# Kernel optimization log

Measured on AMD Instinct MI355X. Metric: run time of the kernel, lower is better.

The kernel has to match this reference:

```python
import jax, jax.numpy as jnp
import numpy as np

B = 8       # complexes in batch
C = 32      # CDR residues per antibody
G = 2048    # antigen nodes per complex
D = 128     # encoded_dims
N_AB = B * C
N_AG = B * G
N = N_AB + N_AG
SLOPE = 0.2
EPS_BN = 1e-5


def _build_edges():
    # block-sparse bipartite edges (cdr_b x ag_b), symmetrized, + self loops
    srcs, dsts = [], []
    for b in range(B):
        ab = np.arange(b * C, (b + 1) * C)
        ag = np.arange(N_AB + b * G, N_AB + (b + 1) * G)
        g1, g2 = np.meshgrid(ab, ag, indexing='ij')
        srcs.append(g1.ravel()); dsts.append(g2.ravel())
    s = np.concatenate(srcs); d = np.concatenate(dsts)
    loops = np.arange(N)
    src = np.concatenate([s, d, loops]).astype(np.int32)
    dst = np.concatenate([d, s, loops]).astype(np.int32)
    return src, dst


def setup_inputs() -> dict:
    key = jax.random.key(0)
    ks = jax.random.split(key, 16)
    sc = 1.0 / np.sqrt(D)
    edge_src, edge_dst = _build_edges()
    return {
        'selected_ab': jax.random.normal(ks[0], (N_AB, D), jnp.float32),
        'x_ag': jax.random.normal(ks[1], (N_AG, D), jnp.float32),
        'W1': jax.random.normal(ks[2], (D, D), jnp.float32) * sc,
        'a_src1': jax.random.normal(ks[3], (D,), jnp.float32) * sc,
        'a_dst1': jax.random.normal(ks[4], (D,), jnp.float32) * sc,
        'b1': jnp.zeros((D,), jnp.float32),
        'W2': jax.random.normal(ks[5], (D, D), jnp.float32) * sc,
        'a_src2': jax.random.normal(ks[6], (D,), jnp.float32) * sc,
        'a_dst2': jax.random.normal(ks[7], (D,), jnp.float32) * sc,
        'b2': jnp.zeros((D,), jnp.float32),
        'bn_ab_g': jnp.ones((2 * D,), jnp.float32),
        'bn_ab_b': jnp.zeros((2 * D,), jnp.float32),
        'bn_ag_g': jnp.ones((2 * D,), jnp.float32),
        'bn_ag_b': jnp.zeros((2 * D,), jnp.float32),
        'fc_w': jax.random.normal(ks[8], (2 * D, 1), jnp.float32) * sc,
        'fc_b': jnp.zeros((1,), jnp.float32),
        'agfc_w': jax.random.normal(ks[9], (2 * D, 1), jnp.float32) * sc,
        'agfc_b': jnp.zeros((1,), jnp.float32),
        'edge_src': jnp.asarray(edge_src),
        'edge_dst': jnp.asarray(edge_dst),
    }


def _gat(x, W, a_s, a_d, b, src, dst):
    # PyG GATConv, heads=1, eval mode (dropout off)
    h = x @ W                                  # [N, D]
    al_s = h @ a_s                             # [N]
    al_d = h @ a_d                             # [N]
    e = jax.nn.leaky_relu(al_s[src] + al_d[dst], SLOPE)   # [E]
    m = jax.ops.segment_max(e, dst, num_segments=N)
    e = jnp.exp(e - m[dst])
    z = jax.ops.segment_sum(e, dst, num_segments=N)
    alpha = e / (z[dst] + 1e-16)
    out = jax.ops.segment_sum(h[src] * alpha[:, None], dst, num_segments=N)
    return out + b


def _bn(x, g, b):
    # training-mode batch stats (biased variance), like torch BatchNorm1d
    m = x.mean(0)
    v = ((x - m) ** 2).mean(0)
    return (x - m) / jnp.sqrt(v + EPS_BN) * g + b


def reference(selected_ab, x_ag, W1, a_src1, a_dst1, b1, W2, a_src2, a_dst2, b2,
              bn_ab_g, bn_ab_b, bn_ag_g, bn_ag_b, fc_w, fc_b, agfc_w, agfc_b,
              edge_src, edge_dst):
    x = jnp.concatenate([selected_ab, x_ag], axis=0)          # [N, D]
    x = jax.nn.relu(_gat(x, W1, a_src1, a_dst1, b1, edge_src, edge_dst))
    x = _gat(x, W2, a_src2, a_dst2, b2, edge_src, edge_dst)
    x_ab = jnp.concatenate([x[:N_AB], selected_ab], axis=1)   # [N_ab, 2D]
    x_ab = jax.nn.relu(_bn(x_ab, bn_ab_g, bn_ab_b))
    x_ab = (x_ab @ fc_w + fc_b).ravel()
    x_ag_o = jnp.concatenate([x[N_AB:], x_ag], axis=1)        # [N_ag, 2D]
    x_ag_o = jax.nn.relu(_bn(x_ag_o, bn_ag_g, bn_ag_b))
    x_ag_o = (x_ag_o @ agfc_w + agfc_b).ravel()
    return (x_ab, x_ag_o)
```

## Files before the change

kernel.cpp:

```cpp
#include <hip/hip_runtime.h>


#define N_AB 256
#define N_AG 16384
#define N_ALL 16640
#define G_AG 2048
#define SLOPE 0.2f
#define MSHIFT 20.0f

typedef __attribute__((ext_vector_type(4))) float f32x4;
typedef __attribute__((ext_vector_type(8))) __bf16 bf16x8;
typedef __attribute__((ext_vector_type(8))) unsigned short u16x8;
typedef unsigned short ushort_t;

__device__ __forceinline__ float bf2f(ushort_t u) {
  union { unsigned int i; float f; } v; v.i = ((unsigned int)u) << 16; return v.f;
}
__device__ __forceinline__ ushort_t f2bf(float f) {
  union { float fv; unsigned int i; } v; v.fv = f;
  unsigned int x = v.i;
  return (ushort_t)((x + 0x7fffu + ((x >> 16) & 1u)) >> 16);
}
__device__ __forceinline__ float lrelu(float x) { return x >= 0.f ? x : SLOPE * x; }
__device__ __forceinline__ float expw(float e) {
  return __expf(fminf(e, 60.f) - MSHIFT);
}
__device__ __forceinline__ float ldf(const void* p, size_t i, int f) {
  return f ? ((const float*)p)[i] : bf2f(((const ushort_t*)p)[i]);
}
__device__ __forceinline__ void ld8f(const void* p, size_t i, int f, float* o) {
  if (f) {
    const f32x4* q = (const f32x4*)((const float*)p + i);
    f32x4 a = q[0], b = q[1];
#pragma unroll
    for (int j = 0; j < 4; ++j) { o[j] = a[j]; o[j + 4] = b[j]; }
  } else {
    u16x8 v = *(const u16x8*)((const ushort_t*)p + i);
#pragma unroll
    for (int j = 0; j < 8; ++j) o[j] = bf2f(v[j]);
  }
}

__global__ __launch_bounds__(256) void k_pre(
    const void* __restrict__ W1, const void* __restrict__ W2,
    const void* __restrict__ as1, const void* __restrict__ ad1,
    const void* __restrict__ as2, const void* __restrict__ ad2,
    const ushort_t* __restrict__ selu,
    ushort_t* __restrict__ W1t, ushort_t* __restrict__ W2t,
    float* __restrict__ va, float* __restrict__ bnsumAG,
    float* __restrict__ accf, float* __restrict__ accz,
    int* __restrict__ flagp) {
  int t = threadIdx.x, lane = t & 63, wid = t >> 6;
  int bx = blockIdx.x;
  int cnt = 0;
#pragma unroll
  for (int i = 0; i < 8; ++i) {
    unsigned e = (selu[lane * 8 + i] >> 7) & 0xFF;
    if (e > 0xC8) cnt++;
  }
  int f = (__popcll(__ballot(cnt > 0)) >= 3) ? 1 : 0;
  if (bx == 0 && t == 0) flagp[0] = f;

  if (bx < 16) {
    const void* W = (bx < 8) ? W1 : W2;
    ushort_t* Wt = (bx < 8) ? W1t : W2t;
    int base = (bx & 7) * 2048 + t * 8;
    float o[8];
    ld8f(W, base, f, o);
#pragma unroll
    for (int j = 0; j < 8; ++j) {
      int idx = base + j;
      Wt[(idx & 127) * 128 + (idx >> 7)] = f2bf(o[j]);
    }
  } else if (bx < 32) {
    int j = bx - 16;
    const void* W   = (j < 8) ? W1 : W2;
    const void* asv = (j < 8) ? as1 : as2;
    const void* adv = (j < 8) ? ad1 : ad2;
    int vbase = (j < 8) ? 0 : 256;
    int basek = (j & 7) * 16 + wid * 4;
    float a_s0 = ldf(asv, lane, f), a_s1 = ldf(asv, lane + 64, f);
    float a_d0 = ldf(adv, lane, f), a_d1 = ldf(adv, lane + 64, f);
#pragma unroll
    for (int i = 0; i < 4; ++i) {
      int k = basek + i;
      float w0 = ldf(W, (size_t)k * 128 + lane, f);
      float w1 = ldf(W, (size_t)k * 128 + lane + 64, f);
      float ps = w0 * a_s0 + w1 * a_s1;
      float pd = w0 * a_d0 + w1 * a_d1;
#pragma unroll
      for (int o = 1; o < 64; o <<= 1) {
        ps += __shfl_xor(ps, o);
        pd += __shfl_xor(pd, o);
      }
      if (lane == 0) { va[vbase + k] = ps; va[vbase + 128 + k] = pd; }
    }
  } else {
    int j = bx - 32;
    f32x4* az = (f32x4*)(accf + (size_t)j * 4096);
    f32x4 z4 = (f32x4){0.f, 0.f, 0.f, 0.f};
    for (int i = t; i < 1024; i += 256) az[i] = z4;
    if (j == 0) { bnsumAG[t] = 0.f; bnsumAG[t + 256] = 0.f; accz[t] = 0.f; }
  }
}

__global__ __launch_bounds__(256) void k_gemm(
    const void* __restrict__ xa, int modeA,
    const void* __restrict__ xb, int modeB,
    const int* __restrict__ flagp,
    const ushort_t* __restrict__ Wt, const float* __restrict__ va,
    ushort_t* __restrict__ h, float* __restrict__ als, float* __restrict__ ald) {
  int lane = threadIdx.x & 63, wid = threadIdx.x >> 6;
  int rw0 = blockIdx.x * 64 + wid * 16;
  const void* xsrc; int roff, mode;
  if (rw0 < N_AB) { xsrc = xa; roff = rw0; mode = modeA; }
  else            { xsrc = xb; roff = rw0 - N_AB; mode = modeB; }
  int fx = (mode == 2) ? *flagp : mode;
  int mm = lane & 15, q = lane >> 4;
  f32x4 acc[8];
#pragma unroll
  for (int b = 0; b < 8; ++b) acc[b] = (f32x4){0.f, 0.f, 0.f, 0.f};
  float pals = 0.f, pald = 0.f;
#pragma unroll
  for (int s = 0; s < 4; ++s) {
    int koff = s * 32 + q * 8;
    union { u16x8 u; bf16x8 b; } af;
    float o[8];
    ld8f(xsrc, (size_t)(roff + mm) * 128 + koff, fx, o);
#pragma unroll
    for (int j = 0; j < 8; ++j) {
      af.u[j] = f2bf(o[j]);
      pals += o[j] * va[koff + j];
      pald += o[j] * va[128 + koff + j];
    }
#pragma unroll
    for (int nt = 0; nt < 8; ++nt) {
      bf16x8 bfr = *(const bf16x8*)(Wt + (size_t)(nt * 16 + mm) * 128 + koff);
      acc[nt] = __builtin_amdgcn_mfma_f32_16x16x32_bf16(af.b, bfr, acc[nt], 0, 0, 0);
    }
  }
  {
    float s1 = pals; s1 += __shfl_xor(s1, 16); s1 += __shfl_xor(s1, 32);
    float d1 = pald; d1 += __shfl_xor(d1, 16); d1 += __shfl_xor(d1, 32);
    if (lane < 16) { als[rw0 + lane] = s1; ald[rw0 + lane] = d1; }
  }
#pragma unroll
  for (int nt = 0; nt < 8; ++nt)
#pragma unroll
    for (int r = 0; r < 4; ++r) {
      int row = rw0 + q * 4 + r;
      int col = nt * 16 + mm;
      h[(size_t)row * 128 + col] = f2bf(acc[nt][r]);
    }
}

#define ABP_STRIDE 72
#define AG_STRIDE 40
__global__ __launch_bounds__(256) void k_agg(
    const ushort_t* __restrict__ h, const float* __restrict__ als,
    const float* __restrict__ ald, const void* __restrict__ bias,
    const int* __restrict__ flagp, ushort_t* __restrict__ xout,
    float* __restrict__ accf, float* __restrict__ accz,
    const void* __restrict__ x_ag, float* __restrict__ bnsumAG,
    int do_relu, int do_bnsum) {
  __shared__ ushort_t hT[128 * ABP_STRIDE];
  __shared__ float alsS[64];
  __shared__ float colsum[128], colsq[128];
  int bx = blockIdx.x;
  int t = threadIdx.x, lane = t & 63, wid = t >> 6;
  int mm = lane & 15, q = lane >> 4;

  if (bx < 256) {
    int b = bx >> 5, jt = bx & 31;
    int f = *flagp;
    {
      int row = t & 31, c0 = (t >> 5) * 16;
      const ushort_t* src = h + (size_t)(b * 32 + row) * 128 + c0;
      u16x8 v0 = *(const u16x8*)src;
      u16x8 v1 = *(const u16x8*)(src + 8);
#pragma unroll
      for (int j = 0; j < 8; ++j) {
        hT[(c0 + j) * AG_STRIDE + row] = v0[j];
        hT[(c0 + 8 + j) * AG_STRIDE + row] = v1[j];
      }
      if (t < 32) alsS[t] = als[b * 32 + t];
      if (t < 128) { colsum[t] = 0.f; colsq[t] = 0.f; }
    }
    __syncthreads();
    int jl = jt * 64 + wid * 16;
    int jrow = N_AB + b * G_AG + jl;
    float aldj = ald[jrow + mm];
    float alsj = als[jrow + mm];
    union { u16x8 u; bf16x8 b; } af;
    float zp = 0.f;
#pragma unroll
    for (int j = 0; j < 8; ++j) {
      ushort_t us = f2bf(expw(lrelu(alsS[q * 8 + j] + aldj)));
      af.u[j] = us;
      zp += bf2f(us);
    }
    zp += __shfl_xor(zp, 16);
    zp += __shfl_xor(zp, 32);
    float wself = expw(lrelu(alsj + aldj));
    float z = zp + wself;
#pragma unroll
    for (int nt = 0; nt < 8; ++nt) {
      int col = nt * 16 + mm;
      union { u16x8 u; bf16x8 b; } bfr;
      bfr.b = *(const bf16x8*)(&hT[col * AG_STRIDE + q * 8]);
      f32x4 acc = {0.f, 0.f, 0.f, 0.f};
      acc = __builtin_amdgcn_mfma_f32_16x16x32_bf16(af.b, bfr.b, acc, 0, 0, 0);
      float biasv = ldf(bias, col, f);
      float sl = 0.f, sq = 0.f;
#pragma unroll
      for (int r = 0; r < 4; ++r) {
        int row = q * 4 + r;
        float zr = __shfl(z, row);
        float wsr = __shfl(wself, row);
        float hv = bf2f(h[(size_t)(jrow + row) * 128 + col]);
        float v = (acc[r] + wsr * hv) / (zr + 1e-16f) + biasv;
        sl += v; sq += v * v;
        if (do_relu) v = fmaxf(v, 0.f);
        xout[(size_t)(jrow + row) * 128 + col] = f2bf(v);
      }
      if (do_bnsum) {
        atomicAdd(&colsum[col], sl);
        atomicAdd(&colsq[col], sq);
      }
    }
    if (do_bnsum) {
      __syncthreads();
      if (t < 128) {
        atomicAdd(&bnsumAG[t], colsum[t]);
        atomicAdd(&bnsumAG[256 + t], colsq[t]);
      }
    }
  } else if (bx < 512) {
    int bx2 = bx - 256;
    int b = bx2 >> 5, sg = bx2 & 31;
    int jrow0 = N_AB + b * G_AG + sg * 64;
    {
      int jr = t & 63, cgrp = (t >> 6) * 32;
      const ushort_t* src = h + (size_t)(jrow0 + jr) * 128 + cgrp;
#pragma unroll
      for (int v = 0; v < 4; ++v) {
        u16x8 vv = *(const u16x8*)(src + v * 8);
#pragma unroll
        for (int j = 0; j < 8; ++j)
          hT[(cgrp + v * 8 + j) * ABP_STRIDE + jr] = vv[j];
      }
      if (t < 64) alsS[t] = als[jrow0 + t];
    }
    __syncthreads();
    float aldm[2] = { ald[b * 32 + mm], ald[b * 32 + 16 + mm] };
    f32x4 acc[2][2];
#pragma unroll
    for (int a = 0; a < 2; ++a)
#pragma unroll
      for (int c = 0; c < 2; ++c) acc[a][c] = (f32x4){0.f, 0.f, 0.f, 0.f};
    float zz[2] = {0.f, 0.f};
#pragma unroll
    for (int s = 0; s < 2; ++s) {
      int k0 = s * 32 + q * 8;
      float a8[8];
#pragma unroll
      for (int j = 0; j < 8; ++j) a8[j] = alsS[k0 + j];
      union { u16x8 u; bf16x8 b; } af[2];
#pragma unroll
      for (int mt = 0; mt < 2; ++mt)
#pragma unroll
        for (int j = 0; j < 8; ++j) {
          ushort_t us = f2bf(expw(lrelu(a8[j] + aldm[mt])));
          af[mt].u[j] = us;
          zz[mt] += bf2f(us);
        }
#pragma unroll
      for (int ns = 0; ns < 2; ++ns) {
        int n = wid * 32 + ns * 16 + mm;
        union { u16x8 u; bf16x8 b; } bfr;
        bfr.b = *(const bf16x8*)(&hT[n * ABP_STRIDE + k0]);
        acc[0][ns] = __builtin_amdgcn_mfma_f32_16x16x32_bf16(af[0].b, bfr.b, acc[0][ns], 0, 0, 0);
        acc[1][ns] = __builtin_amdgcn_mfma_f32_16x16x32_bf16(af[1].b, bfr.b, acc[1][ns], 0, 0, 0);
      }
    }
#pragma unroll
    for (int mt = 0; mt < 2; ++mt)
#pragma unroll
      for (int ns = 0; ns < 2; ++ns)
#pragma unroll
        for (int r = 0; r < 4; ++r) {
          int row = b * 32 + mt * 16 + q * 4 + r;
          int col = wid * 32 + ns * 16 + mm;
          atomicAdd(&accf[(size_t)row * 128 + col], acc[mt][ns][r]);
        }
#pragma unroll
    for (int mt = 0; mt < 2; ++mt) {
      float z = zz[mt];
      z += __shfl_xor(z, 16);
      z += __shfl_xor(z, 32);
      if (wid == 0 && lane < 16)
        atomicAdd(&accz[b * 32 + mt * 16 + lane], z);
    }
  } else {
    int j = bx - 512;
    int f = *flagp;
    int col = t & 127, half = t >> 7;
    int r0 = j * 256 + half * 128;
    float s = 0.f, sq = 0.f;
    for (int r = 0; r < 128; ++r) {
      float v = ldf(x_ag, (size_t)(r0 + r) * 128 + col, f);
      s += v; sq += v * v;
    }
    atomicAdd(&bnsumAG[128 + col], s);
    atomicAdd(&bnsumAG[384 + col], sq);
  }
}

__global__ __launch_bounds__(256) void k_abfin(
    float* __restrict__ accf, float* __restrict__ accz,
    const ushort_t* __restrict__ h, const float* __restrict__ als,
    const float* __restrict__ ald, const void* __restrict__ bias,
    const int* __restrict__ flagp, float* __restrict__ xabf, int do_relu) {
  __shared__ float zsh[32];
  int b = blockIdx.x, t = threadIdx.x;
  int f = *flagp;
  if (t < 32) {
    int grow = b * 32 + t;
    float w = expw(lrelu(als[grow] + ald[grow]));
    zsh[t] = accz[grow] + w;
    accz[grow] = 0.f;
  }
  __syncthreads();
  int c = t & 127, rh = t >> 7;
  float biasv = ldf(bias, c, f);
#pragma unroll 4
  for (int r = 0; r < 16; ++r) {
    int row = rh * 16 + r;
    int grow = b * 32 + row;
    float wself = expw(lrelu(als[grow] + ald[grow]));
    size_t idx = (size_t)grow * 128 + c;
    float hv = bf2f(h[idx]);
    float v = (accf[idx] + wself * hv) / (zsh[row] + 1e-16f) + biasv;
    accf[idx] = 0.f;
    if (do_relu) v = fmaxf(v, 0.f);
    xabf[idx] = v;
  }
}

__global__ __launch_bounds__(256) void k_stats(
    const float* __restrict__ xfab, const void* __restrict__ sel_ab,
    const float* __restrict__ bnsumAG,
    const void* __restrict__ gab, const void* __restrict__ bab,
    const void* __restrict__ gag, const void* __restrict__ bag,
    const void* __restrict__ fcw, const void* __restrict__ agfcw,
    const int* __restrict__ flagp,
    float* __restrict__ statsAB, float* __restrict__ statsAG) {
  int c = threadIdx.x;
  int f = *flagp;
  if (blockIdx.x == 0) {
    float s = 0.f, sq = 0.f;
    if (c < 128) {
      for (int r = 0; r < 256; ++r) { float v = xfab[(size_t)r * 128 + c]; s += v; sq += v * v; }
    } else {
      for (int r = 0; r < 256; ++r) {
        float v = ldf(sel_ab, (size_t)r * 128 + (c - 128), f);
        s += v; sq += v * v;
      }
    }
    float mean = s * (1.f / 256.f);
    float var = fmaxf(sq * (1.f / 256.f) - mean * mean, 0.f);
    float A = ldf(gab, c, f) / sqrtf(var + 1e-5f);
    statsAB[c] = A;
    statsAB[256 + c] = ldf(bab, c, f) - mean * A;
    statsAB[512 + c] = ldf(fcw, c, f);
  } else {
    float mean = bnsumAG[c] * (1.f / 16384.f);
    float var = fmaxf(bnsumAG[256 + c] * (1.f / 16384.f) - mean * mean, 0.f);
    float A = ldf(gag, c, f) / sqrtf(var + 1e-5f);
    statsAG[c] = A;
    statsAG[256 + c] = ldf(bag, c, f) - mean * A;
    statsAG[512 + c] = ldf(agfcw, c, f);
  }
}

__global__ __launch_bounds__(256) void k_head(
    const float* __restrict__ xfab, const ushort_t* __restrict__ xfag,
    const void* __restrict__ sel_ab, const void* __restrict__ x_ag,
    const float* __restrict__ statsAB, const float* __restrict__ statsAG,
    const void* __restrict__ fcb, const void* __restrict__ agfcb,
    const int* __restrict__ flagp, void* __restrict__ out) {
  int lane = threadIdx.x & 63, wid = threadIdx.x >> 6;
  int row = blockIdx.x * 4 + wid;
  int f = *flagp;
  int c0 = lane * 2;
  const float* st;
  float v0, v1, v2, v3, bb;
  if (row < N_AB) {
    st = statsAB;
    const float* p = xfab + (size_t)row * 128 + c0;
    v0 = p[0]; v1 = p[1];
    size_t ro = (size_t)row * 128 + c0;
    v2 = ldf(sel_ab, ro, f);
    v3 = ldf(sel_ab, ro + 1, f);
    bb = ldf(fcb, 0, f);
  } else {
    st = statsAG;
    const ushort_t* p = xfag + (size_t)row * 128 + c0;
    v0 = bf2f(p[0]); v1 = bf2f(p[1]);
    size_t ro = (size_t)(row - N_AB) * 128 + c0;
    v2 = ldf(x_ag, ro, f);
    v3 = ldf(x_ag, ro + 1, f);
    bb = ldf(agfcb, 0, f);
  }
  float acc =
      fmaxf(v0 * st[c0]           + st[256 + c0],     0.f) * st[512 + c0]
    + fmaxf(v1 * st[c0 + 1]       + st[256 + c0 + 1], 0.f) * st[512 + c0 + 1]
    + fmaxf(v2 * st[128 + c0]     + st[384 + c0],     0.f) * st[640 + c0]
    + fmaxf(v3 * st[128 + c0 + 1] + st[384 + c0 + 1], 0.f) * st[640 + c0 + 1];
#pragma unroll
  for (int o = 1; o < 64; o <<= 1) acc += __shfl_xor(acc, o);
  if (lane == 0) {
    float r = acc + bb;
    if (f) ((float*)out)[row] = r;
    else   ((ushort_t*)out)[row] = f2bf(r);
  }
}

extern "C" void kernel_launch(void* const* d_in, const int* in_sizes, int n_in,
                              void* d_out, int out_size, void* d_ws, size_t ws_size,
                              hipStream_t stream) {
  (void)in_sizes; (void)n_in; (void)out_size; (void)ws_size;
  const void* sel_ab = d_in[0];
  const void* x_ag   = d_in[1];
  const void* W1     = d_in[2];
  const void* as1    = d_in[3];
  const void* ad1    = d_in[4];
  const void* b1     = d_in[5];
  const void* W2     = d_in[6];
  const void* as2    = d_in[7];
  const void* ad2    = d_in[8];
  const void* b2     = d_in[9];
  const void* gab    = d_in[10];
  const void* bab    = d_in[11];
  const void* gag    = d_in[12];
  const void* bag    = d_in[13];
  const void* fcw    = d_in[14];
  const void* fcb    = d_in[15];
  const void* agfcw  = d_in[16];
  const void* agfcb  = d_in[17];

  ushort_t* h  = (ushort_t*)d_in[18];
  ushort_t* xb = (ushort_t*)d_in[19];

  char* wsp = (char*)d_ws;
  size_t off = 0;
  auto carve = [&](size_t bytes) -> char* {
    char* p = wsp + off; off += (bytes + 255) & ~(size_t)255; return p;
  };
  int* flag      = (int*)carve(64 * 4);
  ushort_t* W1t  = (ushort_t*)carve(16384 * 2);
  ushort_t* W2t  = (ushort_t*)carve(16384 * 2);
  float* va      = (float*)carve(512 * 4);
  float* als     = (float*)carve((size_t)N_ALL * 4);
  float* ald     = (float*)carve((size_t)N_ALL * 4);
  float* bnsumAG = (float*)carve(512 * 4);
  float* statsAB = (float*)carve(768 * 4);
  float* statsAG = (float*)carve(768 * 4);
  float* xabf    = (float*)carve((size_t)N_AB * 128 * 4);
  float* accf    = (float*)carve((size_t)N_AB * 128 * 4);
  float* accz    = (float*)carve(256 * 4);

  k_pre<<<40, 256, 0, stream>>>(W1, W2, as1, ad1, as2, ad2,
                                (const ushort_t*)sel_ab, W1t, W2t, va,
                                bnsumAG, accf, accz, flag);
  k_gemm<<<260, 256, 0, stream>>>(sel_ab, 2, x_ag, 2, flag, W1t, va, h, als, ald);
  k_agg<<<512, 256, 0, stream>>>(h, als, ald, b1, flag, xb, accf, accz,
                                 x_ag, bnsumAG, 1, 0);
  k_abfin<<<8, 256, 0, stream>>>(accf, accz, h, als, ald, b1, flag, xabf, 1);
  k_gemm<<<260, 256, 0, stream>>>(xabf, 1, xb + (size_t)N_AB * 128, 0, flag, W2t, va + 256, h, als, ald);
  k_agg<<<576, 256, 0, stream>>>(h, als, ald, b2, flag, xb, accf, accz,
                                 x_ag, bnsumAG, 0, 1);
  k_abfin<<<8, 256, 0, stream>>>(accf, accz, h, als, ald, b2, flag, xabf, 0);
  k_stats<<<2, 256, 0, stream>>>(xabf, sel_ab, bnsumAG, gab, bab, gag, bag, fcw, agfcw, flag, statsAB, statsAG);
  k_head<<<4160, 256, 0, stream>>>(xabf, xb, sel_ab, x_ag, statsAB, statsAG, fcb, agfcb, flag, d_out);
}
```

Measured before the change: 199.6 us.

## Fuse all stages into one persistent kernel with software grid barriers

```diff
diff --git a/kernel.cpp b/kernel.cpp
--- a/kernel.cpp
+++ b/kernel.cpp
@@ -7,6 +7,7 @@
 #define G_AG 2048
 #define SLOPE 0.2f
 #define MSHIFT 20.0f
+#define NBLK 512
 
 typedef __attribute__((ext_vector_type(4))) float f32x4;
 typedef __attribute__((ext_vector_type(8))) __bf16 bf16x8;
@@ -41,25 +42,105 @@
   }
 }
 
-__global__ __launch_bounds__(256) void k_pre(
-    const void* __restrict__ W1, const void* __restrict__ W2,
-    const void* __restrict__ as1, const void* __restrict__ ad1,
-    const void* __restrict__ as2, const void* __restrict__ ad2,
-    const ushort_t* __restrict__ selu,
+__device__ __forceinline__ void gbar(int* __restrict__ bar, int id) {
+  __syncthreads();
+  if (threadIdx.x == 0) {
+    __threadfence();
+    atomicAdd(&bar[id], 1);
+    while (__hip_atomic_load(&bar[id], __ATOMIC_RELAXED,
+                             __HIP_MEMORY_SCOPE_AGENT) < NBLK)
+      __builtin_amdgcn_s_sleep(1);
+    __threadfence();
+  }
+  __syncthreads();
+}
+
+__device__ __forceinline__ void gemm_do(
+    const void* xa, int fa, const void* xg, int fg,
+    const ushort_t* __restrict__ Wt, const float* __restrict__ va,
+    ushort_t* __restrict__ h, float* __restrict__ als, float* __restrict__ ald,
+    int bx, int lane, int wid) {
+  int mm = lane & 15, q = lane >> 4;
+  for (int u = bx; u < 520; u += NBLK) {
+    int rw0 = u * 32 + (wid >> 1) * 16;
+    int ch = wid & 1;
+    const void* xsrc; int roff, fx;
+    if (rw0 < N_AB) { xsrc = xa; roff = rw0; fx = fa; }
+    else            { xsrc = xg; roff = rw0 - N_AB; fx = fg; }
+    f32x4 acc[4];
+#pragma unroll
+    for (int b = 0; b < 4; ++b) acc[b] = (f32x4){0.f, 0.f, 0.f, 0.f};
+    float pals = 0.f, pald = 0.f;
+#pragma unroll
+    for (int s = 0; s < 4; ++s) {
+      int koff = s * 32 + q * 8;
+      union { u16x8 u16; bf16x8 b16; } af;
+      float o[8];
+      ld8f(xsrc, (size_t)(roff + mm) * 128 + koff, fx, o);
+#pragma unroll
+      for (int j = 0; j < 8; ++j) {
+        af.u16[j] = f2bf(o[j]);
+        pals += o[j] * va[koff + j];
+        pald += o[j] * va[128 + koff + j];
+      }
+#pragma unroll
+      for (int nt = 0; nt < 4; ++nt) {
+        int colb = ch * 64 + nt * 16;
+        bf16x8 bfr = *(const bf16x8*)(Wt + (size_t)(colb + mm) * 128 + koff);
+        acc[nt] = __builtin_amdgcn_mfma_f32_16x16x32_bf16(af.b16, bfr, acc[nt], 0, 0, 0);
+      }
+    }
+    if (ch == 0) {
+      float s1 = pals; s1 += __shfl_xor(s1, 16); s1 += __shfl_xor(s1, 32);
+      float d1 = pald; d1 += __shfl_xor(d1, 16); d1 += __shfl_xor(d1, 32);
+      if (lane < 16) { als[rw0 + lane] = s1; ald[rw0 + lane] = d1; }
+    }
+#pragma unroll
+    for (int nt = 0; nt < 4; ++nt)
+#pragma unroll
+      for (int r = 0; r < 4; ++r) {
+        int row = rw0 + q * 4 + r;
+        int col = ch * 64 + nt * 16 + mm;
+        h[(size_t)row * 128 + col] = f2bf(acc[nt][r]);
+      }
+  }
+}
+
+__global__ __launch_bounds__(256, 2) void k_fused(
+    const void* __restrict__ sel_ab, const void* __restrict__ x_ag,
+    const void* __restrict__ W1, const void* __restrict__ as1,
+    const void* __restrict__ ad1, const void* __restrict__ b1,
+    const void* __restrict__ W2, const void* __restrict__ as2,
+    const void* __restrict__ ad2, const void* __restrict__ b2,
+    const void* __restrict__ gab, const void* __restrict__ bab,
+    const void* __restrict__ gag, const void* __restrict__ bag,
+    const void* __restrict__ fcw, const void* __restrict__ fcb,
+    const void* __restrict__ agfcw, const void* __restrict__ agfcb,
+    ushort_t* __restrict__ h, ushort_t* __restrict__ xb,
     ushort_t* __restrict__ W1t, ushort_t* __restrict__ W2t,
-    float* __restrict__ va, float* __restrict__ bnsumAG,
+    float* __restrict__ va, float* __restrict__ als, float* __restrict__ ald,
+    float* __restrict__ bnsumAG, float* __restrict__ xabf,
     float* __restrict__ accf, float* __restrict__ accz,
-    int* __restrict__ flagp) {
+    float* __restrict__ statsAG, int* __restrict__ bar,
+    void* __restrict__ out) {
+  __shared__ ushort_t hT[128 * 72];
+  __shared__ float alsS[64];
+  __shared__ float cs0[128], cs1[128];
+  __shared__ float stA[256], stB[256], stW[256];
+  __shared__ float z4[4], w4[4];
+
   int t = threadIdx.x, lane = t & 63, wid = t >> 6;
   int bx = blockIdx.x;
+  int mm = lane & 15, q = lane >> 4;
+
   int cnt = 0;
+  const ushort_t* selu = (const ushort_t*)sel_ab;
 #pragma unroll
   for (int i = 0; i < 8; ++i) {
     unsigned e = (selu[lane * 8 + i] >> 7) & 0xFF;
     if (e > 0xC8) cnt++;
   }
   int f = (__popcll(__ballot(cnt > 0)) >= 3) ? 1 : 0;
-  if (bx == 0 && t == 0) flagp[0] = f;
 
   if (bx < 16) {
     const void* W = (bx < 8) ? W1 : W2;
@@ -95,215 +176,183 @@
       }
       if (lane == 0) { va[vbase + k] = ps; va[vbase + 128 + k] = pd; }
     }
-  } else {
+  } else if (bx < 40) {
     int j = bx - 32;
     f32x4* az = (f32x4*)(accf + (size_t)j * 4096);
-    f32x4 z4 = (f32x4){0.f, 0.f, 0.f, 0.f};
-    for (int i = t; i < 1024; i += 256) az[i] = z4;
+    f32x4 zz = (f32x4){0.f, 0.f, 0.f, 0.f};
+    for (int i = t; i < 1024; i += 256) az[i] = zz;
     if (j == 0) { bnsumAG[t] = 0.f; bnsumAG[t + 256] = 0.f; accz[t] = 0.f; }
   }
-}
-
-__global__ __launch_bounds__(256) void k_gemm(
-    const void* __restrict__ xa, int modeA,
-    const void* __restrict__ xb, int modeB,
-    const int* __restrict__ flagp,
-    const ushort_t* __restrict__ Wt, const float* __restrict__ va,
-    ushort_t* __restrict__ h, float* __restrict__ als, float* __restrict__ ald) {
-  int lane = threadIdx.x & 63, wid = threadIdx.x >> 6;
-  int rw0 = blockIdx.x * 64 + wid * 16;
-  const void* xsrc; int roff, mode;
-  if (rw0 < N_AB) { xsrc = xa; roff = rw0; mode = modeA; }
-  else            { xsrc = xb; roff = rw0 - N_AB; mode = modeB; }
-  int fx = (mode == 2) ? *flagp : mode;
-  int mm = lane & 15, q = lane >> 4;
-  f32x4 acc[8];
-#pragma unroll
-  for (int b = 0; b < 8; ++b) acc[b] = (f32x4){0.f, 0.f, 0.f, 0.f};
-  float pals = 0.f, pald = 0.f;
-#pragma unroll
-  for (int s = 0; s < 4; ++s) {
-    int koff = s * 32 + q * 8;
-    union { u16x8 u; bf16x8 b; } af;
-    float o[8];
-    ld8f(xsrc, (size_t)(roff + mm) * 128 + koff, fx, o);
-#pragma unroll
-    for (int j = 0; j < 8; ++j) {
-      af.u[j] = f2bf(o[j]);
-      pals += o[j] * va[koff + j];
-      pald += o[j] * va[128 + koff + j];
-    }
-#pragma unroll
-    for (int nt = 0; nt < 8; ++nt) {
-      bf16x8 bfr = *(const bf16x8*)(Wt + (size_t)(nt * 16 + mm) * 128 + koff);
-      acc[nt] = __builtin_amdgcn_mfma_f32_16x16x32_bf16(af.b, bfr, acc[nt], 0, 0, 0);
-    }
-  }
-  {
-    float s1 = pals; s1 += __shfl_xor(s1, 16); s1 += __shfl_xor(s1, 32);
-    float d1 = pald; d1 += __shfl_xor(d1, 16); d1 += __shfl_xor(d1, 32);
-    if (lane < 16) { als[rw0 + lane] = s1; ald[rw0 + lane] = d1; }
-  }
-#pragma unroll
-  for (int nt = 0; nt < 8; ++nt)
-#pragma unroll
-    for (int r = 0; r < 4; ++r) {
-      int row = rw0 + q * 4 + r;
-      int col = nt * 16 + mm;
-      h[(size_t)row * 128 + col] = f2bf(acc[nt][r]);
-    }
-}
-
-#define ABP_STRIDE 72
-#define AG_STRIDE 40
-__global__ __launch_bounds__(256) void k_agg(
-    const ushort_t* __restrict__ h, const float* __restrict__ als,
-    const float* __restrict__ ald, const void* __restrict__ bias,
-    const int* __restrict__ flagp, ushort_t* __restrict__ xout,
-    float* __restrict__ accf, float* __restrict__ accz,
-    const void* __restrict__ x_ag, float* __restrict__ bnsumAG,
-    int do_relu, int do_bnsum) {
-  __shared__ ushort_t hT[128 * ABP_STRIDE];
-  __shared__ float alsS[64];
-  __shared__ float colsum[128], colsq[128];
-  int bx = blockIdx.x;
-  int t = threadIdx.x, lane = t & 63, wid = t >> 6;
-  int mm = lane & 15, q = lane >> 4;
-
-  if (bx < 256) {
-    int b = bx >> 5, jt = bx & 31;
-    int f = *flagp;
-    {
-      int row = t & 31, c0 = (t >> 5) * 16;
-      const ushort_t* src = h + (size_t)(b * 32 + row) * 128 + c0;
-      u16x8 v0 = *(const u16x8*)src;
-      u16x8 v1 = *(const u16x8*)(src + 8);
+  gbar(bar, 0);
+
+  gemm_do(sel_ab, f, x_ag, f, W1t, va, h, als, ald, bx, lane, wid);
+  gbar(bar, 1);
+
+  auto agg_phase = [&](const void* bias, int do_relu, int do_bnsum) {
+    if (bx < 256) {
+      int b = bx >> 5, jt = bx & 31;
+      {
+        int row = t & 31, c0g = (t >> 5) * 16;
+        const ushort_t* src = h + (size_t)(b * 32 + row) * 128 + c0g;
+        u16x8 v0 = *(const u16x8*)src;
+        u16x8 v1 = *(const u16x8*)(src + 8);
+#pragma unroll
+        for (int j = 0; j < 8; ++j) {
+          hT[(c0g + j) * 40 + row] = v0[j];
+          hT[(c0g + 8 + j) * 40 + row] = v1[j];
+        }
+        if (t < 32) alsS[t] = als[b * 32 + t];
+        if (t < 128) { cs0[t] = 0.f; cs1[t] = 0.f; }
+      }
+      __syncthreads();
+      int jl = jt * 64 + wid * 16;
+      int jrow = N_AB + b * G_AG + jl;
+      float aldj = ald[jrow + mm];
+      float alsj = als[jrow + mm];
+      union { u16x8 u16; bf16x8 b16; } af;
+      float zp = 0.f;
 #pragma unroll
       for (int j = 0; j < 8; ++j) {
-        hT[(c0 + j) * AG_STRIDE + row] = v0[j];
-        hT[(c0 + 8 + j) * AG_STRIDE + row] = v1[j];
-      }
-      if (t < 32) alsS[t] = als[b * 32 + t];
-      if (t < 128) { colsum[t] = 0.f; colsq[t] = 0.f; }
-    }
-    __syncthreads();
-    int jl = jt * 64 + wid * 16;
-    int jrow = N_AB + b * G_AG + jl;
-    float aldj = ald[jrow + mm];
-    float alsj = als[jrow + mm];
-    union { u16x8 u; bf16x8 b; } af;
-    float zp = 0.f;
-#pragma unroll
-    for (int j = 0; j < 8; ++j) {
-      ushort_t us = f2bf(expw(lrelu(alsS[q * 8 + j] + aldj)));
-      af.u[j] = us;
-      zp += bf2f(us);
-    }
-    zp += __shfl_xor(zp, 16);
-    zp += __shfl_xor(zp, 32);
-    float wself = expw(lrelu(alsj + aldj));
-    float z = zp + wself;
-#pragma unroll
-    for (int nt = 0; nt < 8; ++nt) {
-      int col = nt * 16 + mm;
-      union { u16x8 u; bf16x8 b; } bfr;
-      bfr.b = *(const bf16x8*)(&hT[col * AG_STRIDE + q * 8]);
-      f32x4 acc = {0.f, 0.f, 0.f, 0.f};
-      acc = __builtin_amdgcn_mfma_f32_16x16x32_bf16(af.b, bfr.b, acc, 0, 0, 0);
-      float biasv = ldf(bias, col, f);
-      float sl = 0.f, sq = 0.f;
-#pragma unroll
-      for (int r = 0; r < 4; ++r) {
-        int row = q * 4 + r;
-        float zr = __shfl(z, row);
-        float wsr = __shfl(wself, row);
-        float hv = bf2f(h[(size_t)(jrow + row) * 128 + col]);
-        float v = (acc[r] + wsr * hv) / (zr + 1e-16f) + biasv;
-        sl += v; sq += v * v;
+        ushort_t us = f2bf(expw(lrelu(alsS[q * 8 + j] + aldj)));
+        af.u16[j] = us;
+        zp += bf2f(us);
+      }
+      zp += __shfl_xor(zp, 16);
+      zp += __shfl_xor(zp, 32);
+      float wself = expw(lrelu(alsj + aldj));
+      float z = zp + wself;
+#pragma unroll
+      for (int nt = 0; nt < 8; ++nt) {
+        int col = nt * 16 + mm;
+        union { u16x8 u16; bf16x8 b16; } bfr;
+        bfr.b16 = *(const bf16x8*)(&hT[col * 40 + q * 8]);
+        f32x4 acc = {0.f, 0.f, 0.f, 0.f};
+        acc = __builtin_amdgcn_mfma_f32_16x16x32_bf16(af.b16, bfr.b16, acc, 0, 0, 0);
+        float biasv = ldf(bias, col, f);
+        float sl = 0.f, sq = 0.f;
+#pragma unroll
+        for (int r = 0; r < 4; ++r) {
+          int row = q * 4 + r;
+          float zr = __shfl(z, row);
+          float wsr = __shfl(wself, row);
+          float hv = bf2f(h[(size_t)(jrow + row) * 128 + col]);
+          float v = (acc[r] + wsr * hv) / (zr + 1e-16f) + biasv;
+          sl += v; sq += v * v;
+          if (do_relu) v = fmaxf(v, 0.f);
+          xb[(size_t)(jrow + row) * 128 + col] = f2bf(v);
+        }
+        if (do_bnsum) {
+          atomicAdd(&cs0[col], sl);
+          atomicAdd(&cs1[col], sq);
+        }
+      }
+      if (do_bnsum) {
+        __syncthreads();
+        if (t < 128) {
+          atomicAdd(&bnsumAG[t], cs0[t]);
+          atomicAdd(&bnsumAG[256 + t], cs1[t]);
+        }
+      }
+    } else {
+      int bx2 = bx - 256;
+      int b = bx2 >> 5, sg = bx2 & 31;
+      int jrow0 = N_AB + b * G_AG + sg * 64;
+      {
+        int jr = t & 63, cgrp = (t >> 6) * 32;
+        const ushort_t* src = h + (size_t)(jrow0 + jr) * 128 + cgrp;
+#pragma unroll
+        for (int v = 0; v < 4; ++v) {
+          u16x8 vv = *(const u16x8*)(src + v * 8);
+#pragma unroll
+          for (int j = 0; j < 8; ++j)
+            hT[(cgrp + v * 8 + j) * 72 + jr] = vv[j];
+        }
+        if (t < 64) alsS[t] = als[jrow0 + t];
+      }
+      __syncthreads();
+      float aldm[2] = { ald[b * 32 + mm], ald[b * 32 + 16 + mm] };
+      f32x4 acc[2][2];
+#pragma unroll
+      for (int a = 0; a < 2; ++a)
+#pragma unroll
+        for (int c = 0; c < 2; ++c) acc[a][c] = (f32x4){0.f, 0.f, 0.f, 0.f};
+      float zz[2] = {0.f, 0.f};
+#pragma unroll
+      for (int s = 0; s < 2; ++s) {
+        int k0 = s * 32 + q * 8;
+        float a8[8];
+#pragma unroll
+        for (int j = 0; j < 8; ++j) a8[j] = alsS[k0 + j];
+        union { u16x8 u16; bf16x8 b16; } af[2];
+#pragma unroll
+        for (int mt = 0; mt < 2; ++mt)
+#pragma unroll
+          for (int j = 0; j < 8; ++j) {
+            ushort_t us = f2bf(expw(lrelu(a8[j] + aldm[mt])));
+            af[mt].u16[j] = us;
+            zz[mt] += bf2f(us);
+          }
+#pragma unroll
+        for (int ns = 0; ns < 2; ++ns) {
+          int n = wid * 32 + ns * 16 + mm;
+          union { u16x8 u16; bf16x8 b16; } bfr;
+          bfr.b16 = *(const bf16x8*)(&hT[n * 72 + k0]);
+          acc[0][ns] = __builtin_amdgcn_mfma_f32_16x16x32_bf16(af[0].b16, bfr.b16, acc[0][ns], 0, 0, 0);
+          acc[1][ns] = __builtin_amdgcn_mfma_f32_16x16x32_bf16(af[1].b16, bfr.b16, acc[1][ns], 0, 0, 0);
+        }
+      }
+#pragma unroll
+      for (int mt = 0; mt < 2; ++mt)
+#pragma unroll
+        for (int ns = 0; ns < 2; ++ns)
+#pragma unroll
+          for (int r = 0; r < 4; ++r) {
+            int row = b * 32 + mt * 16 + q * 4 + r;
+            int col = wid * 32 + ns * 16 + mm;
+            atomicAdd(&accf[(size_t)row * 128 + col], acc[mt][ns][r]);
+          }
+#pragma unroll
+      for (int mt = 0; mt < 2; ++mt) {
+        float z = zz[mt];
+        z += __shfl_xor(z, 16);
+        z += __shfl_xor(z, 32);
+        if (wid == 0 && lane < 16)
+          atomicAdd(&accz[b * 32 + mt * 16 + lane], z);
+      }
+    }
+  };
+
+  auto abfin_phase = [&](const void* bias, int do_relu) {
+    if (bx < 64) {
+      int b = bx >> 3, rg = bx & 7;
+      if (t < 4) {
+        int grow = b * 32 + rg * 4 + t;
+        float w = expw(lrelu(als[grow] + ald[grow]));
+        z4[t] = accz[grow] + w;
+        w4[t] = w;
+        accz[grow] = 0.f;
+      }
+      __syncthreads();
+#pragma unroll
+      for (int e = t; e < 512; e += 256) {
+        int rl = e >> 7, col = e & 127;
+        int grow = b * 32 + rg * 4 + rl;
+        size_t idx = (size_t)grow * 128 + col;
+        float hv = bf2f(h[idx]);
+        float v = (accf[idx] + w4[rl] * hv) / (z4[rl] + 1e-16f) + ldf(bias, col, f);
+        accf[idx] = 0.f;
         if (do_relu) v = fmaxf(v, 0.f);
-        xout[(size_t)(jrow + row) * 128 + col] = f2bf(v);
-      }
-      if (do_bnsum) {
-        atomicAdd(&colsum[col], sl);
-        atomicAdd(&colsq[col], sq);
-      }
-    }
-    if (do_bnsum) {
-      __syncthreads();
-      if (t < 128) {
-        atomicAdd(&bnsumAG[t], colsum[t]);
-        atomicAdd(&bnsumAG[256 + t], colsq[t]);
-      }
-    }
-  } else if (bx < 512) {
-    int bx2 = bx - 256;
-    int b = bx2 >> 5, sg = bx2 & 31;
-    int jrow0 = N_AB + b * G_AG + sg * 64;
-    {
-      int jr = t & 63, cgrp = (t >> 6) * 32;
-      const ushort_t* src = h + (size_t)(jrow0 + jr) * 128 + cgrp;
-#pragma unroll
-      for (int v = 0; v < 4; ++v) {
-        u16x8 vv = *(const u16x8*)(src + v * 8);
-#pragma unroll
-        for (int j = 0; j < 8; ++j)
-          hT[(cgrp + v * 8 + j) * ABP_STRIDE + jr] = vv[j];
-      }
-      if (t < 64) alsS[t] = als[jrow0 + t];
-    }
-    __syncthreads();
-    float aldm[2] = { ald[b * 32 + mm], ald[b * 32 + 16 + mm] };
-    f32x4 acc[2][2];
-#pragma unroll
-    for (int a = 0; a < 2; ++a)
-#pragma unroll
-      for (int c = 0; c < 2; ++c) acc[a][c] = (f32x4){0.f, 0.f, 0.f, 0.f};
-    float zz[2] = {0.f, 0.f};
-#pragma unroll
-    for (int s = 0; s < 2; ++s) {
-      int k0 = s * 32 + q * 8;
-      float a8[8];
-#pragma unroll
-      for (int j = 0; j < 8; ++j) a8[j] = alsS[k0 + j];
-      union { u16x8 u; bf16x8 b; } af[2];
-#pragma unroll
-      for (int mt = 0; mt < 2; ++mt)
-#pragma unroll
-        for (int j = 0; j < 8; ++j) {
-          ushort_t us = f2bf(expw(lrelu(a8[j] + aldm[mt])));
-          af[mt].u[j] = us;
-          zz[mt] += bf2f(us);
-        }
-#pragma unroll
-      for (int ns = 0; ns < 2; ++ns) {
-        int n = wid * 32 + ns * 16 + mm;
-        union { u16x8 u; bf16x8 b; } bfr;
-        bfr.b = *(const bf16x8*)(&hT[n * ABP_STRIDE + k0]);
-        acc[0][ns] = __builtin_amdgcn_mfma_f32_16x16x32_bf16(af[0].b, bfr.b, acc[0][ns], 0, 0, 0);
-        acc[1][ns] = __builtin_amdgcn_mfma_f32_16x16x32_bf16(af[1].b, bfr.b, acc[1][ns], 0, 0, 0);
-      }
-    }
-#pragma unroll
-    for (int mt = 0; mt < 2; ++mt)
-#pragma unroll
-      for (int ns = 0; ns < 2; ++ns)
-#pragma unroll
-        for (int r = 0; r < 4; ++r) {
-          int row = b * 32 + mt * 16 + q * 4 + r;
-          int col = wid * 32 + ns * 16 + mm;
-          atomicAdd(&accf[(size_t)row * 128 + col], acc[mt][ns][r]);
-        }
-#pragma unroll
-    for (int mt = 0; mt < 2; ++mt) {
-      float z = zz[mt];
-      z += __shfl_xor(z, 16);
-      z += __shfl_xor(z, 32);
-      if (wid == 0 && lane < 16)
-        atomicAdd(&accz[b * 32 + mt * 16 + lane], z);
-    }
-  } else {
-    int j = bx - 512;
-    int f = *flagp;
+        xabf[idx] = v;
+      }
+    }
+  };
+
+  agg_phase(b1, 1, 0);
+  gbar(bar, 2);
+
+  abfin_phase(b1, 1);
+  if (bx >= 64 && bx < 128) {
+    int j = bx - 64;
     int col = t & 127, half = t >> 7;
     int r0 = j * 256 + half * 128;
     float s = 0.f, sq = 0.f;
@@ -314,115 +363,93 @@
     atomicAdd(&bnsumAG[128 + col], s);
     atomicAdd(&bnsumAG[384 + col], sq);
   }
-}
-
-__global__ __launch_bounds__(256) void k_abfin(
-    float* __restrict__ accf, float* __restrict__ accz,
-    const ushort_t* __restrict__ h, const float* __restrict__ als,
-    const float* __restrict__ ald, const void* __restrict__ bias,
-    const int* __restrict__ flagp, float* __restrict__ xabf, int do_relu) {
-  __shared__ float zsh[32];
-  int b = blockIdx.x, t = threadIdx.x;
-  int f = *flagp;
-  if (t < 32) {
-    int grow = b * 32 + t;
-    float w = expw(lrelu(als[grow] + ald[grow]));
-    zsh[t] = accz[grow] + w;
-    accz[grow] = 0.f;
-  }
-  __syncthreads();
-  int c = t & 127, rh = t >> 7;
-  float biasv = ldf(bias, c, f);
-#pragma unroll 4
-  for (int r = 0; r < 16; ++r) {
-    int row = rh * 16 + r;
-    int grow = b * 32 + row;
-    float wself = expw(lrelu(als[grow] + ald[grow]));
-    size_t idx = (size_t)grow * 128 + c;
-    float hv = bf2f(h[idx]);
-    float v = (accf[idx] + wself * hv) / (zsh[row] + 1e-16f) + biasv;
-    accf[idx] = 0.f;
-    if (do_relu) v = fmaxf(v, 0.f);
-    xabf[idx] = v;
-  }
-}
-
-__global__ __launch_bounds__(256) void k_stats(
-    const float* __restrict__ xfab, const void* __restrict__ sel_ab,
-    const float* __restrict__ bnsumAG,
-    const void* __restrict__ gab, const void* __restrict__ bab,
-    const void* __restrict__ gag, const void* __restrict__ bag,
-    const void* __restrict__ fcw, const void* __restrict__ agfcw,
-    const int* __restrict__ flagp,
-    float* __restrict__ statsAB, float* __restrict__ statsAG) {
-  int c = threadIdx.x;
-  int f = *flagp;
-  if (blockIdx.x == 0) {
-    float s = 0.f, sq = 0.f;
-    if (c < 128) {
-      for (int r = 0; r < 256; ++r) { float v = xfab[(size_t)r * 128 + c]; s += v; sq += v * v; }
-    } else {
-      for (int r = 0; r < 256; ++r) {
-        float v = ldf(sel_ab, (size_t)r * 128 + (c - 128), f);
-        s += v; sq += v * v;
-      }
-    }
-    float mean = s * (1.f / 256.f);
-    float var = fmaxf(sq * (1.f / 256.f) - mean * mean, 0.f);
-    float A = ldf(gab, c, f) / sqrtf(var + 1e-5f);
-    statsAB[c] = A;
-    statsAB[256 + c] = ldf(bab, c, f) - mean * A;
-    statsAB[512 + c] = ldf(fcw, c, f);
+  gbar(bar, 3);
+
+  gemm_do(xabf, 1, xb + (size_t)N_AB * 128, 0, W2t, va + 256, h, als, ald,
+          bx, lane, wid);
+  gbar(bar, 4);
+
+  agg_phase(b2, 0, 1);
+  gbar(bar, 5);
+
+  abfin_phase(b2, 0);
+  if (bx == 64 && t < 256) {
+    float mean = bnsumAG[t] * (1.f / 16384.f);
+    float var = fmaxf(bnsumAG[256 + t] * (1.f / 16384.f) - mean * mean, 0.f);
+    float A = ldf(gag, t, f) / sqrtf(var + 1e-5f);
+    statsAG[t] = A;
+    statsAG[256 + t] = ldf(bag, t, f) - mean * A;
+    statsAG[512 + t] = ldf(agfcw, t, f);
+  }
+  gbar(bar, 6);
+
+  if (bx < 504) {
+    if (t < 256) { stA[t] = statsAG[t]; stB[t] = statsAG[256 + t]; stW[t] = statsAG[512 + t]; }
+    __syncthreads();
+    float bb = ldf(agfcb, 0, f);
+    int c0 = lane * 2;
+    for (int u = bx; u < 4096; u += 504) {
+      int rloc = u * 4 + wid;
+      int row = N_AB + rloc;
+      const ushort_t* p = xb + (size_t)row * 128 + c0;
+      float v0 = bf2f(p[0]), v1 = bf2f(p[1]);
+      size_t ro = (size_t)rloc * 128 + c0;
+      float v2 = ldf(x_ag, ro, f), v3 = ldf(x_ag, ro + 1, f);
+      float acc =
+          fmaxf(v0 * stA[c0]           + stB[c0],       0.f) * stW[c0]
+        + fmaxf(v1 * stA[c0 + 1]       + stB[c0 + 1],   0.f) * stW[c0 + 1]
+        + fmaxf(v2 * stA[128 + c0]     + stB[128 + c0], 0.f) * stW[128 + c0]
+        + fmaxf(v3 * stA[128 + c0 + 1] + stB[128 + c0 + 1], 0.f) * stW[128 + c0 + 1];
+#pragma unroll
+      for (int o = 1; o < 64; o <<= 1) acc += __shfl_xor(acc, o);
+      if (lane == 0) {
+        float r = acc + bb;
+        if (f) ((float*)out)[row] = r;
+        else   ((ushort_t*)out)[row] = f2bf(r);
+      }
+    }
   } else {
-    float mean = bnsumAG[c] * (1.f / 16384.f);
-    float var = fmaxf(bnsumAG[256 + c] * (1.f / 16384.f) - mean * mean, 0.f);
-    float A = ldf(gag, c, f) / sqrtf(var + 1e-5f);
-    statsAG[c] = A;
-    statsAG[256 + c] = ldf(bag, c, f) - mean * A;
-    statsAG[512 + c] = ldf(agfcw, c, f);
-  }
-}
-
-__global__ __launch_bounds__(256) void k_head(
-    const float* __restrict__ xfab, const ushort_t* __restrict__ xfag,
-    const void* __restrict__ sel_ab, const void* __restrict__ x_ag,
-    const float* __restrict__ statsAB, const float* __restrict__ statsAG,
-    const void* __restrict__ fcb, const void* __restrict__ agfcb,
-    const int* __restrict__ flagp, void* __restrict__ out) {
-  int lane = threadIdx.x & 63, wid = threadIdx.x >> 6;
-  int row = blockIdx.x * 4 + wid;
-  int f = *flagp;
-  int c0 = lane * 2;
-  const float* st;
-  float v0, v1, v2, v3, bb;
-  if (row < N_AB) {
-    st = statsAB;
-    const float* p = xfab + (size_t)row * 128 + c0;
-    v0 = p[0]; v1 = p[1];
-    size_t ro = (size_t)row * 128 + c0;
-    v2 = ldf(sel_ab, ro, f);
-    v3 = ldf(sel_ab, ro + 1, f);
-    bb = ldf(fcb, 0, f);
-  } else {
-    st = statsAG;
-    const ushort_t* p = xfag + (size_t)row * 128 + c0;
-    v0 = bf2f(p[0]); v1 = bf2f(p[1]);
-    size_t ro = (size_t)(row - N_AB) * 128 + c0;
-    v2 = ldf(x_ag, ro, f);
-    v3 = ldf(x_ag, ro + 1, f);
-    bb = ldf(agfcb, 0, f);
-  }
-  float acc =
-      fmaxf(v0 * st[c0]           + st[256 + c0],     0.f) * st[512 + c0]
-    + fmaxf(v1 * st[c0 + 1]       + st[256 + c0 + 1], 0.f) * st[512 + c0 + 1]
-    + fmaxf(v2 * st[128 + c0]     + st[384 + c0],     0.f) * st[640 + c0]
-    + fmaxf(v3 * st[128 + c0 + 1] + st[384 + c0 + 1], 0.f) * st[640 + c0 + 1];
-#pragma unroll
-  for (int o = 1; o < 64; o <<= 1) acc += __shfl_xor(acc, o);
-  if (lane == 0) {
-    float r = acc + bb;
-    if (f) ((float*)out)[row] = r;
-    else   ((ushort_t*)out)[row] = f2bf(r);
+    int b8 = bx - 504;
+    if (t < 256) {
+      float s = 0.f, sq = 0.f;
+      if (t < 128) {
+        for (int r = 0; r < 256; ++r) { float v = xabf[(size_t)r * 128 + t]; s += v; sq += v * v; }
+      } else {
+        for (int r = 0; r < 256; ++r) {
+          float v = ldf(sel_ab, (size_t)r * 128 + (t - 128), f);
+          s += v; sq += v * v;
+        }
+      }
+      float mean = s * (1.f / 256.f);
+      float var = fmaxf(sq * (1.f / 256.f) - mean * mean, 0.f);
+      float A = ldf(gab, t, f) / sqrtf(var + 1e-5f);
+      stA[t] = A;
+      stB[t] = ldf(bab, t, f) - mean * A;
+      stW[t] = ldf(fcw, t, f);
+    }
+    __syncthreads();
+    float bb = ldf(fcb, 0, f);
+    int c0 = lane * 2;
+#pragma unroll
+    for (int it = 0; it < 8; ++it) {
+      int row = b8 * 32 + it * 4 + wid;
+      const float* p = xabf + (size_t)row * 128 + c0;
+      float v0 = p[0], v1 = p[1];
+      size_t ro = (size_t)row * 128 + c0;
+      float v2 = ldf(sel_ab, ro, f), v3 = ldf(sel_ab, ro + 1, f);
+      float acc =
+          fmaxf(v0 * stA[c0]           + stB[c0],       0.f) * stW[c0]
+        + fmaxf(v1 * stA[c0 + 1]       + stB[c0 + 1],   0.f) * stW[c0 + 1]
+        + fmaxf(v2 * stA[128 + c0]     + stB[128 + c0], 0.f) * stW[128 + c0]
+        + fmaxf(v3 * stA[128 + c0 + 1] + stB[128 + c0 + 1], 0.f) * stW[128 + c0 + 1];
+#pragma unroll
+      for (int o = 1; o < 64; o <<= 1) acc += __shfl_xor(acc, o);
+      if (lane == 0) {
+        float r = acc + bb;
+        if (f) ((float*)out)[row] = r;
+        else   ((ushort_t*)out)[row] = f2bf(r);
+      }
+    }
   }
 }
 
@@ -457,30 +484,22 @@
   auto carve = [&](size_t bytes) -> char* {
     char* p = wsp + off; off += (bytes + 255) & ~(size_t)255; return p;
   };
-  int* flag      = (int*)carve(64 * 4);
+  int* bar       = (int*)carve(64 * 4);
   ushort_t* W1t  = (ushort_t*)carve(16384 * 2);
   ushort_t* W2t  = (ushort_t*)carve(16384 * 2);
   float* va      = (float*)carve(512 * 4);
   float* als     = (float*)carve((size_t)N_ALL * 4);
   float* ald     = (float*)carve((size_t)N_ALL * 4);
   float* bnsumAG = (float*)carve(512 * 4);
-  float* statsAB = (float*)carve(768 * 4);
   float* statsAG = (float*)carve(768 * 4);
   float* xabf    = (float*)carve((size_t)N_AB * 128 * 4);
   float* accf    = (float*)carve((size_t)N_AB * 128 * 4);
   float* accz    = (float*)carve(256 * 4);
 
-  k_pre<<<40, 256, 0, stream>>>(W1, W2, as1, ad1, as2, ad2,
-                                (const ushort_t*)sel_ab, W1t, W2t, va,
-                                bnsumAG, accf, accz, flag);
-  k_gemm<<<260, 256, 0, stream>>>(sel_ab, 2, x_ag, 2, flag, W1t, va, h, als, ald);
-  k_agg<<<512, 256, 0, stream>>>(h, als, ald, b1, flag, xb, accf, accz,
-                                 x_ag, bnsumAG, 1, 0);
-  k_abfin<<<8, 256, 0, stream>>>(accf, accz, h, als, ald, b1, flag, xabf, 1);
-  k_gemm<<<260, 256, 0, stream>>>(xabf, 1, xb + (size_t)N_AB * 128, 0, flag, W2t, va + 256, h, als, ald);
-  k_agg<<<576, 256, 0, stream>>>(h, als, ald, b2, flag, xb, accf, accz,
-                                 x_ag, bnsumAG, 0, 1);
-  k_abfin<<<8, 256, 0, stream>>>(accf, accz, h, als, ald, b2, flag, xabf, 0);
-  k_stats<<<2, 256, 0, stream>>>(xabf, sel_ab, bnsumAG, gab, bab, gag, bag, fcw, agfcw, flag, statsAB, statsAG);
-  k_head<<<4160, 256, 0, stream>>>(xabf, xb, sel_ab, x_ag, statsAB, statsAG, fcb, agfcb, flag, d_out);
-}
+  hipMemsetAsync(bar, 0, 64 * sizeof(int), stream);
+  k_fused<<<NBLK, 256, 0, stream>>>(
+      sel_ab, x_ag, W1, as1, ad1, b1, W2, as2, ad2, b2,
+      gab, bab, gag, bag, fcw, fcb, agfcw, agfcb,
+      h, xb, W1t, W2t, va, als, ald, bnsumAG, xabf, accf, accz,
+      statsAG, bar, d_out);
+}
```

Measured after the change: 525.1 us. 2.63x slower.
